# Kernel optimization log

Measured on AMD Instinct MI355X. Metric: run time of the kernel, lower is better.

## Reference

```python
import jax, jax.numpy as jnp
import numpy as np

NUM_BINS = 16
D_MODEL = 128
TAIL_BOUND = 20.0
MIN_BIN_WIDTH = 1e-3
MIN_BIN_HEIGHT = 1e-3
MIN_DERIVATIVE = 1e-3
EPS = 1e-6


def setup_inputs() -> dict:
    key = jax.random.key(0)
    ks = jax.random.split(key, 10)
    B, S = 32, 8192
    sc = 0.05  # small init scale so spline logits stay moderate
    return {
        "inputs": jax.random.normal(ks[0], (B, S), dtype=jnp.float32),
        "conditioning": jax.random.normal(ks[1], (B, S, D_MODEL), dtype=jnp.float32),
        "Ww": jax.random.normal(ks[2], (NUM_BINS, D_MODEL), dtype=jnp.float32) * sc,
        "bw": jax.random.normal(ks[3], (NUM_BINS,), dtype=jnp.float32) * sc,
        "Wh": jax.random.normal(ks[4], (NUM_BINS, D_MODEL), dtype=jnp.float32) * sc,
        "bh": jax.random.normal(ks[5], (NUM_BINS,), dtype=jnp.float32) * sc,
        "Wd": jax.random.normal(ks[6], (NUM_BINS - 1, D_MODEL), dtype=jnp.float32) * sc,
        "bd": jax.random.normal(ks[7], (NUM_BINS - 1,), dtype=jnp.float32) * sc,
        "Wl": jax.random.normal(ks[8], (NUM_BINS, D_MODEL), dtype=jnp.float32) * sc,
        "bl": jax.random.normal(ks[9], (NUM_BINS,), dtype=jnp.float32) * sc,
    }


def _rational_linear_spline(x, uw, uh, ud, ul, left, right, bottom, top):
    nb = uw.shape[-1]
    # bin widths / cumulative widths
    w = MIN_BIN_WIDTH + (1.0 - MIN_BIN_WIDTH * nb) * jax.nn.softmax(uw, axis=-1)
    cw = jnp.concatenate([jnp.zeros_like(w[..., :1]), jnp.cumsum(w, axis=-1)], axis=-1)
    cw = (right - left) * cw + left
    cw = cw.at[..., 0].set(left).at[..., -1].set(right)
    w = cw[..., 1:] - cw[..., :-1]
    # derivatives (ud already padded to nb+1 by caller)
    d = MIN_DERIVATIVE + jax.nn.softplus(ud)
    # bin heights / cumulative heights
    h = MIN_BIN_HEIGHT + (1.0 - MIN_BIN_HEIGHT * nb) * jax.nn.softmax(uh, axis=-1)
    ch = jnp.concatenate([jnp.zeros_like(h[..., :1]), jnp.cumsum(h, axis=-1)], axis=-1)
    ch = (top - bottom) * ch + bottom
    ch = ch.at[..., 0].set(bottom).at[..., -1].set(top)
    h = ch[..., 1:] - ch[..., :-1]
    # searchsorted via sum of comparisons (as in source)
    locs = cw.at[..., -1].add(EPS)
    idx = jnp.sum((x[..., None] >= locs).astype(jnp.int32), axis=-1) - 1
    idx = jnp.clip(idx, 0, nb - 1)
    g = lambda t: jnp.take_along_axis(t, idx[..., None], axis=-1)[..., 0]
    in_cw = g(cw)
    in_bw = g(w)
    in_ch = g(ch)
    in_delta = g(h / w)
    dk = g(d)
    dk1 = g(d[..., 1:])
    in_h = g(h)
    lambdas = 0.95 * jax.nn.sigmoid(ul) + 0.025
    lam = g(lambdas)
    wa = 1.0
    wb = jnp.sqrt(dk / dk1) * wa
    wc = (lam * wa * dk + (1.0 - lam) * wb * dk1) / in_delta
    ya = in_ch
    yb = in_h + in_ch
    yc = ((1.0 - lam) * wa * ya + lam * wb * yb) / ((1.0 - lam) * wa + lam * wb)
    theta = (x - in_cw) / in_bw
    m = theta <= lam
    num = jnp.where(m, wa * ya * (lam - theta) + wc * yc * theta,
                    wc * yc * (1.0 - theta) + wb * yb * (theta - lam))
    den = jnp.where(m, wa * (lam - theta) + wc * theta,
                    wc * (1.0 - theta) + wb * (theta - lam))
    out = num / den
    deriv_num = jnp.where(m, wa * wc * lam * (yc - ya), wb * wc * (1.0 - lam) * (yb - yc)) / in_bw
    logabsdet = jnp.log(deriv_num) - 2.0 * jnp.log(jnp.abs(den))
    return out, logabsdet


def reference(inputs, conditioning, Ww, bw, Wh, bh, Wd, bd, Wl, bl):
    # parameter nets (module.forward): note the module normalizes here AND the
    # spline normalizes again -- replicate faithfully.
    uw = jax.nn.softmax(jnp.einsum('bsd,kd->bsk', conditioning, Ww) + bw, axis=-1)
    uh = jax.nn.softmax(jnp.einsum('bsd,kd->bsk', conditioning, Wh) + bh, axis=-1)
    ud = jax.nn.softplus(jnp.einsum('bsd,kd->bsk', conditioning, Wd) + bd)
    ul = jax.nn.sigmoid(jnp.einsum('bsd,kd->bsk', conditioning, Wl) + bl)
    # linear tails: pad derivatives with constant so boundary derivative == 1
    const = float(np.log(np.exp(1.0 - MIN_DERIVATIVE) - 1.0))
    edge = jnp.full(ud.shape[:-1] + (1,), const, dtype=ud.dtype)
    udp = jnp.concatenate([edge, ud, edge], axis=-1)  # [B,S,nb+1]
    tb = TAIL_BOUND
    inside = (inputs >= -tb) & (inputs <= tb)
    xc = jnp.clip(inputs, -tb, tb)
    s_out, s_lad = _rational_linear_spline(xc, uw, uh, udp, ul, -tb, tb, -tb, tb)
    outputs = jnp.where(inside, s_out, inputs)
    logabsdet = jnp.where(inside, s_lad, 0.0)
    return outputs, logabsdet
```

## Files before the change

### kernel.cpp

```cpp
#include <hip/hip_runtime.h>
#include <math.h>

#define NB 16
#define DM 128
#define BM 256
#define ZSTRIDE 68

typedef _Float16 half8  __attribute__((ext_vector_type(8)));
typedef _Float16 half4v __attribute__((ext_vector_type(4)));
typedef _Float16 half2v __attribute__((ext_vector_type(2)));
typedef __fp16   fp16x2 __attribute__((ext_vector_type(2)));
typedef float    f32x4  __attribute__((ext_vector_type(4)));

__device__ __forceinline__ float frcp_(float x) { return __builtin_amdgcn_rcpf(x); }
__device__ __forceinline__ float softplus_fast(float x) {
    return fmaxf(x, 0.0f) + __logf(1.0f + __expf(-fabsf(x)));
}
__device__ __forceinline__ float sigmoid_fast(float x) {
    return frcp_(1.0f + __expf(-x));
}
__device__ __forceinline__ void softmax16_m(float* z) {
    float m = z[0];
#pragma unroll
    for (int k = 1; k < NB; k++) m = fmaxf(m, z[k]);
    float s = 0.0f;
#pragma unroll
    for (int k = 0; k < NB; k++) { z[k] = __expf(z[k] - m); s += z[k]; }
    float r = frcp_(s);
#pragma unroll
    for (int k = 0; k < NB; k++) z[k] *= r;
}
__device__ __forceinline__ void softmax16_nm(float* z) {
    float s = 0.0f;
#pragma unroll
    for (int k = 0; k < NB; k++) { z[k] = __expf(z[k]); s += z[k]; }
    float r = frcp_(s);
#pragma unroll
    for (int k = 0; k < NB; k++) z[k] *= r;
}

__device__ __forceinline__ half2v pk_(float lo, float hi) {
    fp16x2 p = __builtin_amdgcn_cvt_pkrtz(lo, hi);
    return __builtin_bit_cast(half2v, p);
}
__device__ __forceinline__ half8 cvt8(float4 a0, float4 a1) {
    half2v p0 = pk_(a0.x, a0.y);
    half2v p1 = pk_(a0.z, a0.w);
    half2v p2 = pk_(a1.x, a1.y);
    half2v p3 = pk_(a1.z, a1.w);
    half8 f;
    f[0] = p0[0]; f[1] = p0[1]; f[2] = p1[0]; f[3] = p1[1];
    f[4] = p2[0]; f[5] = p2[1]; f[6] = p3[0]; f[7] = p3[1];
    return f;
}

#define LOADC(P, cr)                                    \
    P##0 = *(const float4*)((cr) + 0);                  \
    P##1 = *(const float4*)((cr) + 16);                 \
    P##2 = *(const float4*)((cr) + 32);                 \
    P##3 = *(const float4*)((cr) + 48);                 \
    P##4 = *(const float4*)((cr) + 64);                 \
    P##5 = *(const float4*)((cr) + 80);                 \
    P##6 = *(const float4*)((cr) + 96);                 \
    P##7 = *(const float4*)((cr) + 112);

#define CVTC(P)                                         \
    af0 = cvt8(P##0, P##1);                             \
    af1 = cvt8(P##2, P##3);                             \
    af2 = cvt8(P##4, P##5);                             \
    af3 = cvt8(P##6, P##7);

#define MFMA_GRP(af, s) {                                                       \
    const half8 bt0 = *(const half8*)(Blds + (((0*4+(s))*64 + lane) * 8));      \
    const half8 bt1 = *(const half8*)(Blds + (((1*4+(s))*64 + lane) * 8));      \
    const half8 bt2 = *(const half8*)(Blds + (((2*4+(s))*64 + lane) * 8));      \
    const half8 bt3 = *(const half8*)(Blds + (((3*4+(s))*64 + lane) * 8));      \
    acc0 = __builtin_amdgcn_mfma_f32_16x16x32_f16(af, bt0, acc0, 0, 0, 0);      \
    acc1 = __builtin_amdgcn_mfma_f32_16x16x32_f16(af, bt1, acc1, 0, 0, 0);      \
    acc2 = __builtin_amdgcn_mfma_f32_16x16x32_f16(af, bt2, acc2, 0, 0, 0);      \
    acc3 = __builtin_amdgcn_mfma_f32_16x16x32_f16(af, bt3, acc3, 0, 0, 0);      \
}

#define STOREZ(c) {                                                             \
    _Float16* zpw = zbase + (size_t)((c) * 16) * ZSTRIDE;                       \
    _Pragma("unroll")                                                           \
    for (int r = 0; r < 4; r++) {                                               \
        half2v p0 = pk_(acc0[r], acc1[r]);                                      \
        half2v p1 = pk_(acc2[r], acc3[r]);                                      \
        half4v w; w[0] = p0[0]; w[1] = p0[1]; w[2] = p1[0]; w[3] = p1[1];       \
        *(half4v*)(zpw + (size_t)r * ZSTRIDE) = w;                              \
    } }

#define RESET_ACC  acc0 = zf4; acc1 = zf4; acc2 = zf4; acc3 = zf4;

#define GEMM_CHUNK(P, c)                                                        \
    CVTC(P)                                                                     \
    MFMA_GRP(af0, 0) MFMA_GRP(af1, 1) MFMA_GRP(af2, 2) MFMA_GRP(af3, 3)         \
    STOREZ(c) RESET_ACC

#define STAGE_B_LDS(Wt, isWd) {                                                 \
    const bool val = (!(isWd)) || (l15 < 15);                                   \
    const float* srcl = (Wt) + (size_t)(val ? l15 : 0) * DM + lg * 4;           \
    float4 q0 = *(const float4*)(srcl + 0),  q1 = *(const float4*)(srcl + 16);  \
    float4 q2 = *(const float4*)(srcl + 32), q3 = *(const float4*)(srcl + 48);  \
    float4 q4 = *(const float4*)(srcl + 64), q5 = *(const float4*)(srcl + 80);  \
    float4 q6 = *(const float4*)(srcl + 96), q7 = *(const float4*)(srcl + 112); \
    half8 Q0 = val ? cvt8(q0, q1) : hz;                                         \
    half8 Q1 = val ? cvt8(q2, q3) : hz;                                         \
    half8 Q2 = val ? cvt8(q4, q5) : hz;                                         \
    half8 Q3 = val ? cvt8(q6, q7) : hz;                                         \
    *(half8*)(Blds + (((wave*4+0)*64 + lane) * 8)) = Q0;                        \
    *(half8*)(Blds + (((wave*4+1)*64 + lane) * 8)) = Q1;                        \
    *(half8*)(Blds + (((wave*4+2)*64 + lane) * 8)) = Q2;                        \
    *(half8*)(Blds + (((wave*4+3)*64 + lane) * 8)) = Q3;                        \
}

#define FENCE_LDS                                       \
    __builtin_amdgcn_sched_barrier(0);                  \
    asm volatile("s_waitcnt lgkmcnt(0)" ::: "memory");  \
    __builtin_amdgcn_sched_barrier(0);

#define CPTR(c) (cond + (((bRow + (size_t)(wave * 64 + (c) * 16 + l15)) < (size_t)N) \
                    ? (bRow + (size_t)(wave * 64 + (c) * 16 + l15))                  \
                    : ((size_t)N - 1)) * DM + lg * 4)

#define EPILOGUE(xv, giv)                                                        \
  if ((giv) < (size_t)N) {                                                       \
    float zw[NB], zh[NB], zl[NB], zd[NB - 1];                                    \
    const half4v* zr4 = (const half4v*)&Z[(size_t)tid * ZSTRIDE];                \
    _Pragma("unroll")                                                            \
    for (int j = 0; j < NB; j++) {                                               \
        half4v v = zr4[j];                                                       \
        zw[j] = (float)v[0] + bw[j];                                             \
        zh[j] = (float)v[1] + bh[j];                                             \
        zl[j] = (float)v[2] + bl[j];                                             \
        if (j < NB - 1) zd[j] = (float)v[3] + bd[j];                             \
    }                                                                            \
    float xc = fminf(fmaxf((xv), -20.0f), 20.0f);                                \
    softmax16_m(zw);                                                             \
    softmax16_nm(zw);                                                            \
    const float scale = (1.0f - 1e-3f * NB);                                     \
    float cw[NB + 1];                                                            \
    cw[0] = -20.0f;                                                              \
    float cum = 0.0f;                                                            \
    _Pragma("unroll")                                                            \
    for (int k = 0; k < NB; k++) {                                               \
        cum += 1e-3f + scale * zw[k];                                            \
        cw[k + 1] = 40.0f * cum - 20.0f;                                         \
    }                                                                            \
    cw[NB] = 20.0f;                                                              \
    softmax16_m(zh);                                                             \
    softmax16_nm(zh);                                                            \
    float ch[NB + 1];                                                            \
    ch[0] = -20.0f;                                                              \
    cum = 0.0f;                                                                  \
    _Pragma("unroll")                                                            \
    for (int k = 0; k < NB; k++) {                                               \
        cum += 1e-3f + scale * zh[k];                                            \
        ch[k + 1] = 40.0f * cum - 20.0f;                                         \
    }                                                                            \
    ch[NB] = 20.0f;                                                              \
    float in_cw = cw[0], cw_hi = cw[1], in_ch = ch[0], ch_hi = ch[1];            \
    float zl_sel = zl[0], zd_lo = zd[0], zd_hi = zd[0];                          \
    _Pragma("unroll")                                                            \
    for (int k = 1; k < NB; k++) {                                               \
        bool take = (xc >= cw[k]);                                               \
        in_cw  = take ? cw[k]     : in_cw;                                       \
        cw_hi  = take ? cw[k + 1] : cw_hi;                                       \
        in_ch  = take ? ch[k]     : in_ch;                                       \
        ch_hi  = take ? ch[k + 1] : ch_hi;                                       \
        zl_sel = take ? zl[k]     : zl_sel;                                      \
        zd_lo  = take ? zd[k - 1] : zd_lo;                                       \
        zd_hi  = take ? zd[(k < NB - 1) ? k : NB - 2] : zd_hi;                   \
    }                                                                            \
    bool firstbin = (xc <  cw[1]);                                               \
    bool lastbin  = (xc >= cw[NB - 1]);                                          \
    float in_bw = cw_hi - in_cw;                                                 \
    float in_h  = ch_hi - in_ch;                                                 \
    float dk  = firstbin ? 1.0f : (1e-3f + softplus_fast(softplus_fast(zd_lo))); \
    float dk1 = lastbin  ? 1.0f : (1e-3f + softplus_fast(softplus_fast(zd_hi))); \
    float ul  = sigmoid_fast(zl_sel);                                            \
    float lam = 0.95f * sigmoid_fast(ul) + 0.025f;                               \
    float rbw = frcp_(in_bw);                                                    \
    float in_delta = in_h * rbw;                                                 \
    float wb = sqrtf(dk * frcp_(dk1));                                           \
    float wc = (lam * dk + (1.0f - lam) * wb * dk1) * frcp_(in_delta);           \
    float ya = in_ch;                                                            \
    float yb = in_h + in_ch;                                                     \
    float yc = ((1.0f - lam) * ya + lam * wb * yb) * frcp_((1.0f - lam) + lam * wb); \
    float theta = (xc - in_cw) * rbw;                                            \
    bool mlt = (theta <= lam);                                                   \
    float num = mlt ? (ya * (lam - theta) + wc * yc * theta)                     \
                    : (wc * yc * (1.0f - theta) + wb * yb * (theta - lam));      \
    float den = mlt ? ((lam - theta) + wc * theta)                               \
                    : (wc * (1.0f - theta) + wb * (theta - lam));                \
    float sout = num * frcp_(den);                                               \
    float dnum = (mlt ? (wc * lam * (yc - ya))                                   \
                      : (wb * wc * (1.0f - lam) * (yb - yc))) * rbw;             \
    float slad = __logf(dnum) - 2.0f * __logf(fabsf(den));                       \
    bool inside = ((xv) >= -20.0f) && ((xv) <= 20.0f);                           \
    out[(giv)] = inside ? sout : (xv);                                           \
    lad[(giv)] = inside ? slad : 0.0f;                                           \
  }

__global__ __launch_bounds__(256, 3) void spline_mfma(
    const float* __restrict__ xin, const float* __restrict__ cond,
    const float* __restrict__ Ww, const float* __restrict__ bw,
    const float* __restrict__ Wh, const float* __restrict__ bh,
    const float* __restrict__ Wd, const float* __restrict__ bd,
    const float* __restrict__ Wl, const float* __restrict__ bl,
    float* __restrict__ out, float* __restrict__ lad, int N)
{
    __shared__ __align__(16) _Float16 Z[BM * ZSTRIDE];
    __shared__ __align__(16) _Float16 Blds[16 * 64 * 8];

    const int tid  = threadIdx.x;
    const int wave = tid >> 6;
    const int lane = tid & 63;
    const int l15  = lane & 15;
    const int lg   = lane >> 4;

    const size_t bRow = (size_t)blockIdx.x * BM;
    const size_t gi = bRow + tid;

    half8 hz;
    hz[0]=hz[1]=hz[2]=hz[3]=hz[4]=hz[5]=hz[6]=hz[7] = (_Float16)0.0f;
    {
        const float* Wt = (wave == 0) ? Ww : (wave == 1) ? Wh : (wave == 2) ? Wl : Wd;
        const bool isWd = (wave == 3);
        STAGE_B_LDS(Wt, isWd)
    }
    __syncthreads();

    float4 A0_0, A0_1, A0_2, A0_3, A0_4, A0_5, A0_6, A0_7;
    float4 A1_0, A1_1, A1_2, A1_3, A1_4, A1_5, A1_6, A1_7;
    float4 A2_0, A2_1, A2_2, A2_3, A2_4, A2_5, A2_6, A2_7;
    float4 A3_0, A3_1, A3_2, A3_3, A3_4, A3_5, A3_6, A3_7;
    LOADC(A0_, CPTR(0))
    LOADC(A1_, CPTR(1))
    LOADC(A2_, CPTR(2))
    LOADC(A3_, CPTR(3))
    float x = xin[gi < (size_t)N ? gi : 0];

    const f32x4 zf4 = {0.f, 0.f, 0.f, 0.f};
    f32x4 acc0 = zf4, acc1 = zf4, acc2 = zf4, acc3 = zf4;
    half8 af0, af1, af2, af3;
    _Float16* zbase = &Z[(size_t)(wave * 64 + lg * 4) * ZSTRIDE + l15 * 4];

    GEMM_CHUNK(A0_, 0)
    GEMM_CHUNK(A1_, 1)
    GEMM_CHUNK(A2_, 2)
    GEMM_CHUNK(A3_, 3)

    FENCE_LDS
    EPILOGUE(x, gi)
}

extern "C" void kernel_launch(void* const* d_in, const int* in_sizes, int n_in,
                              void* d_out, int out_size, void* d_ws, size_t ws_size,
                              hipStream_t stream) {
    const float* xin  = (const float*)d_in[0];
    const float* cond = (const float*)d_in[1];
    const float* Ww   = (const float*)d_in[2];
    const float* bwp  = (const float*)d_in[3];
    const float* Wh   = (const float*)d_in[4];
    const float* bhp  = (const float*)d_in[5];
    const float* Wd   = (const float*)d_in[6];
    const float* bdp  = (const float*)d_in[7];
    const float* Wl   = (const float*)d_in[8];
    const float* blp  = (const float*)d_in[9];
    int N = in_sizes[0];
    float* out = (float*)d_out;
    float* lad = out + N;
    int grid = (N + BM - 1) / BM;
    hipLaunchKernelGGL(spline_mfma, dim3(grid), dim3(256), 0, stream,
                       xin, cond, Ww, bwp, Wh, bhp, Wd, bdp, Wl, blp, out, lad, N);
}
```

Before: 33.50 us.

## Process two tiles per block, prefetching the second tile during the epilogue

Each block now handles two 256-row tiles, tile t0 and t0+gridDim, and the grid is halved. Part of the second tile's conditioning rows is loaded before the first tile's epilogue runs, so global-memory latency overlaps with the transcendental-heavy spline math. The weight staging into LDS is also amortized over two tiles. The cost is more live registers and fewer blocks in flight, which could lower occupancy or spill. Reusing the Z LDS buffer without a barrier between tiles may also be a hazard.

After: 33.78 us. Within noise of the previous version (+0.8%).

```diff
diff --git a/kernel.cpp b/kernel.cpp
--- a/kernel.cpp
+++ b/kernel.cpp
@@ -120,8 +120,8 @@
     asm volatile("s_waitcnt lgkmcnt(0)" ::: "memory");  \
     __builtin_amdgcn_sched_barrier(0);
 
-#define CPTR(c) (cond + (((bRow + (size_t)(wave * 64 + (c) * 16 + l15)) < (size_t)N) \
-                    ? (bRow + (size_t)(wave * 64 + (c) * 16 + l15))                  \
+#define CPTR(t, c) (cond + ((((size_t)(t) * BM + (size_t)(wave * 64 + (c) * 16 + l15)) < (size_t)N) \
+                    ? ((size_t)(t) * BM + (size_t)(wave * 64 + (c) * 16 + l15))                     \
                     : ((size_t)N - 1)) * DM + lg * 4)
 
 #define EPILOGUE(xv, giv)                                                        \
@@ -220,8 +220,10 @@
     const int l15  = lane & 15;
     const int lg   = lane >> 4;
 
-    const size_t bRow = (size_t)blockIdx.x * BM;
-    const size_t gi = bRow + tid;
+    const int nTiles = (N + BM - 1) / BM;
+    const int t0 = (int)blockIdx.x;
+    const int t1 = t0 + (int)gridDim.x;
+    const bool hasT1 = (t1 < nTiles);
 
     half8 hz;
     hz[0]=hz[1]=hz[2]=hz[3]=hz[4]=hz[5]=hz[6]=hz[7] = (_Float16)0.0f;
@@ -232,15 +234,18 @@
     }
     __syncthreads();
 
+    const size_t gi0 = (size_t)t0 * BM + tid;
+    const size_t gi1 = (size_t)t1 * BM + tid;
+
     float4 A0_0, A0_1, A0_2, A0_3, A0_4, A0_5, A0_6, A0_7;
     float4 A1_0, A1_1, A1_2, A1_3, A1_4, A1_5, A1_6, A1_7;
     float4 A2_0, A2_1, A2_2, A2_3, A2_4, A2_5, A2_6, A2_7;
     float4 A3_0, A3_1, A3_2, A3_3, A3_4, A3_5, A3_6, A3_7;
-    LOADC(A0_, CPTR(0))
-    LOADC(A1_, CPTR(1))
-    LOADC(A2_, CPTR(2))
-    LOADC(A3_, CPTR(3))
-    float x = xin[gi < (size_t)N ? gi : 0];
+    LOADC(A0_, CPTR(t0, 0))
+    LOADC(A1_, CPTR(t0, 1))
+    LOADC(A2_, CPTR(t0, 2))
+    LOADC(A3_, CPTR(t0, 3))
+    float x0 = xin[gi0 < (size_t)N ? gi0 : 0];
 
     const f32x4 zf4 = {0.f, 0.f, 0.f, 0.f};
     f32x4 acc0 = zf4, acc1 = zf4, acc2 = zf4, acc3 = zf4;
@@ -252,8 +257,26 @@
     GEMM_CHUNK(A2_, 2)
     GEMM_CHUNK(A3_, 3)
 
+    float x1 = 0.0f;
+    if (hasT1) {
+        LOADC(A0_, CPTR(t1, 0))
+        LOADC(A1_, CPTR(t1, 1))
+        x1 = xin[gi1 < (size_t)N ? gi1 : 0];
+    }
+
     FENCE_LDS
-    EPILOGUE(x, gi)
+    EPILOGUE(x0, gi0)
+
+    if (hasT1) {
+        LOADC(A2_, CPTR(t1, 2))
+        LOADC(A3_, CPTR(t1, 3))
+        GEMM_CHUNK(A0_, 0)
+        GEMM_CHUNK(A1_, 1)
+        GEMM_CHUNK(A2_, 2)
+        GEMM_CHUNK(A3_, 3)
+        FENCE_LDS
+        EPILOGUE(x1, gi1)
+    }
 }
 
 extern "C" void kernel_launch(void* const* d_in, const int* in_sizes, int n_in,
@@ -272,7 +295,8 @@
     int N = in_sizes[0];
     float* out = (float*)d_out;
     float* lad = out + N;
-    int grid = (N + BM - 1) / BM;
+    int nTiles = (N + BM - 1) / BM;
+    int grid = (nTiles + 1) / 2;
     hipLaunchKernelGGL(spline_mfma, dim3(grid), dim3(256), 0, stream,
                        xin, cond, Ww, bwp, Wh, bhp, Wd, bdp, Wl, blp, out, lad, N);
 }
```
